# Performance work log

Hardware: AMD Instinct MI355X
Metric: run time of the kernel (lower is better)

Reference implementation:

```python
import jax, jax.numpy as jnp
import numpy as np


def setup_inputs() -> dict:
    key = jax.random.key(0)
    ks = jax.random.split(key, 12)
    B, S, D = 2, 1024, 1024       # batch, seq_len, hidden
    DF_S, DF_E, E = 2048, 512, 8   # shared ffn, expert ffn, n_experts
    W = 0.02                       # weight init scale
    x = jax.random.normal(ks[0], (B, S, D), jnp.float32)
    router_weight = jax.random.normal(ks[1], (E, D), jnp.float32) * W
    sh_gate_w = jax.random.normal(ks[2], (DF_S, D), jnp.float32) * W
    sh_up_w = jax.random.normal(ks[3], (DF_S, D), jnp.float32) * W
    sh_down_w = jax.random.normal(ks[4], (D, DF_S), jnp.float32) * W
    gate_q = jax.random.randint(ks[5], (E, DF_E, D), -128, 128, jnp.int32)
    up_q = jax.random.randint(ks[6], (E, DF_E, D), -128, 128, jnp.int32)
    down_q = jax.random.randint(ks[7], (E, D, DF_E), -128, 128, jnp.int32)
    gate_s = jax.random.uniform(ks[8], (E, DF_E), jnp.float32) * 0.001
    up_s = jax.random.uniform(ks[9], (E, DF_E), jnp.float32) * 0.001
    down_s = jax.random.uniform(ks[10], (E, D), jnp.float32) * 0.001
    alpha = 0.5 + jax.random.uniform(ks[11], (E,), jnp.float32)  # effective_alpha per expert
    return dict(x=x, router_weight=router_weight, sh_gate_w=sh_gate_w,
                sh_up_w=sh_up_w, sh_down_w=sh_down_w, gate_s=gate_s,
                up_s=up_s, down_s=down_s, alpha=alpha, gate_q=gate_q,
                up_q=up_q, down_q=down_q, top_k=2)


def reference(x, router_weight, sh_gate_w, sh_up_w, sh_down_w,
              gate_s, up_s, down_s, alpha, gate_q, up_q, down_q, top_k):
    B, S, D = x.shape
    T = B * S
    E = router_weight.shape[0]
    xf = x.reshape(T, D).astype(jnp.float32)
    # shared SwiGLU MLP
    shared = (jax.nn.silu(xf @ sh_gate_w.T) * (xf @ sh_up_w.T)) @ sh_down_w.T  # [T, D]
    # router: top-k + softmax over selected logits
    logits = xf @ router_weight.T                                # [T, E]
    k = min(int(top_k), E)
    vals, idx = jax.lax.top_k(logits, k)
    w = jax.nn.softmax(vals, axis=-1)                            # [T, k]
    # scatter routing weights into dense combine matrix [T, E] (topk idx are distinct)
    combine = jnp.zeros((T, E), jnp.float32).at[jnp.arange(T)[:, None], idx].add(w)
    # on-the-fly dequantization: int8-range quants * per-row scale
    gw = gate_q.astype(jnp.float32) * gate_s[..., None]          # [E, DF_E, D]
    uw = up_q.astype(jnp.float32) * up_s[..., None]              # [E, DF_E, D]
    dw = down_q.astype(jnp.float32) * down_s[..., None]          # [E, D, DF_E]
    # expert SwiGLU for every (token, expert) pair, combined by routing weights
    g = jnp.einsum('td,efd->tef', xf, gw)                        # [T, E, DF_E]
    u = jnp.einsum('td,efd->tef', xf, uw)
    eo = jnp.einsum('tef,edf->ted', jax.nn.silu(g) * u, dw)      # [T, E, D]
    delta = eo - shared[:, None, :]                              # expert output minus shared
    mixed = shared + jnp.einsum('te,ted->td', combine * alpha[None, :], delta)
    return mixed.reshape(B, S, D)
```

## Files before the change

kernel.cpp:

```cpp
#include <hip/hip_runtime.h>
#include <math.h>

#define T_TOK 2048
#define D_DIM 1024
#define E_NUM 8
#define DFS   2048
#define DFE   512

#define BK 32

typedef short short8 __attribute__((ext_vector_type(8)));
typedef float floatx4 __attribute__((ext_vector_type(4)));
typedef unsigned short ushort;

__device__ __forceinline__ ushort f2b(float f) {
  union { float f; unsigned u; } v; v.f = f;
  unsigned r = (v.u + 0x7fffu + ((v.u >> 16) & 1u)) >> 16;
  return (ushort)r;
}

__device__ __forceinline__ void gld16(const ushort* g, ushort* l) {
  __builtin_amdgcn_global_load_lds(
      (const __attribute__((address_space(1))) void*)g,
      (__attribute__((address_space(3))) void*)l,
      16, 0, 0);
}

__device__ __forceinline__ float silu_mul(float g, float u) {
  return (g / (1.f + __expf(-g))) * u;
}

__global__ __launch_bounds__(256) void mega_prep(
    const float* __restrict__ x, const float* __restrict__ rw,
    const float* __restrict__ alpha,
    const float* __restrict__ sg, const float* __restrict__ su,
    const float* __restrict__ sd,
    const int* __restrict__ gq, const int* __restrict__ uq,
    const int* __restrict__ dq,
    int* __restrict__ choice, float2* __restrict__ cpair,
    float* __restrict__ csum, ushort* __restrict__ xb,
    ushort* __restrict__ sgb, ushort* __restrict__ subb,
    ushort* __restrict__ sdb,
    ushort* __restrict__ gqb, ushort* __restrict__ uqb,
    ushort* __restrict__ dqb) {
  const int b = blockIdx.x;
  const int tid = threadIdx.x;
  if (b < 512) {
    __shared__ float xs[4 * D_DIM];
    const size_t base = (size_t)b * 4 * D_DIM;
#pragma unroll
    for (int j = 0; j < 4; ++j) {
      const int idx = j * 1024 + tid * 4;
      float4 v = *(const float4*)(x + base + idx);
      *(float4*)&xs[idx] = v;
      union { ushort u[4]; uint2 p; } o;
      o.u[0] = f2b(v.x); o.u[1] = f2b(v.y); o.u[2] = f2b(v.z); o.u[3] = f2b(v.w);
      *(uint2*)(xb + base + idx) = o.p;
    }
    __syncthreads();
    const int w = tid >> 6, l = tid & 63;
    const int t = b * 4 + w;
    const int e = l >> 3, sub = l & 7;
    const float* wr = rw + e * D_DIM;
    float acc = 0.f;
#pragma unroll
    for (int k = 0; k < 32; ++k) {
      const int d = k * 32 + sub * 4;
      float4 xv = *(const float4*)&xs[w * D_DIM + d];
      float4 wv = *(const float4*)(wr + d);
      acc += xv.x * wv.x + xv.y * wv.y + xv.z * wv.z + xv.w * wv.w;
    }
    acc += __shfl_xor(acc, 1);
    acc += __shfl_xor(acc, 2);
    acc += __shfl_xor(acc, 4);
    float lg[8];
#pragma unroll
    for (int i = 0; i < 8; ++i) lg[i] = __shfl(acc, i * 8);
    if (l == 0) {
      int i0 = 0; float v0 = lg[0];
#pragma unroll
      for (int i = 1; i < E_NUM; ++i) if (lg[i] > v0) { v0 = lg[i]; i0 = i; }
      int i1 = -1; float v1 = -1e30f;
#pragma unroll
      for (int i = 0; i < E_NUM; ++i) {
        if (i == i0) continue;
        if (lg[i] > v1) { v1 = lg[i]; i1 = i; }
      }
      float w0 = 1.f / (1.f + __expf(v1 - v0));
      float w1 = 1.f - w0;
      float c0 = w0 * alpha[i0];
      float c1 = w1 * alpha[i1];
      csum[t] = c0 + c1;
      choice[t] = i0 | (i1 << 4);
      cpair[t] = make_float2(c0, c1);
    }
  } else if (b < 512 + 3072) {
    const int bb = b - 512;
    const int which = bb >> 10;
    const float* src; ushort* dst;
    if (which == 0) { src = sg; dst = sgb; }
    else if (which == 1) { src = su; dst = subb; }
    else { src = sd; dst = sdb; }
    const size_t i = (size_t)(bb & 1023) * 256 + tid;
    const float4* sp = (const float4*)src;
    float4 a = sp[2 * i], c = sp[2 * i + 1];
    union { ushort u[8]; uint4 v; } o;
    o.u[0] = f2b(a.x); o.u[1] = f2b(a.y); o.u[2] = f2b(a.z); o.u[3] = f2b(a.w);
    o.u[4] = f2b(c.x); o.u[5] = f2b(c.y); o.u[6] = f2b(c.z); o.u[7] = f2b(c.w);
    ((uint4*)dst)[i] = o.v;
  } else {
    const int bb = b - 3584;
    const int which = bb >> 11;
    const int* src; ushort* dst;
    if (which == 0) { src = gq; dst = gqb; }
    else if (which == 1) { src = uq; dst = uqb; }
    else { src = dq; dst = dqb; }
    const size_t i = (size_t)(bb & 2047) * 256 + tid;
    const int4* sp = (const int4*)src;
    int4 a = sp[2 * i], c = sp[2 * i + 1];
    union { ushort u[8]; uint4 v; } o;
    o.u[0] = f2b((float)a.x); o.u[1] = f2b((float)a.y);
    o.u[2] = f2b((float)a.z); o.u[3] = f2b((float)a.w);
    o.u[4] = f2b((float)c.x); o.u[5] = f2b((float)c.y);
    o.u[6] = f2b((float)c.z); o.u[7] = f2b((float)c.w);
    ((uint4*)dst)[i] = o.v;
  }
}

__global__ __launch_bounds__(1024) void build_lists(
    const int* __restrict__ choice, int* __restrict__ cnt,
    int* __restrict__ tok_list, uint2* __restrict__ ass) {
  __shared__ int lcnt[E_NUM];
  __shared__ int lbase[E_NUM];
  const int tid = threadIdx.x;
  if (tid < E_NUM) lcnt[tid] = 0;
  __syncthreads();
  uint2 tmp[T_TOK / 1024];
#pragma unroll
  for (int r = 0; r < T_TOK / 1024; ++r) {
    const int t = r * 1024 + tid;
    const int ch = choice[t];
    const int i0 = ch & 15, i1 = ch >> 4;
    const int p0 = atomicAdd(&lcnt[i0], 1);
    tok_list[i0 * T_TOK + p0] = t;
    const int p1 = atomicAdd(&lcnt[i1], 1);
    tok_list[i1 * T_TOK + p1] = t;
    tmp[r] = make_uint2((unsigned)((i0 << 16) | p0), (unsigned)((i1 << 16) | p1));
  }
  __syncthreads();
  if (tid < E_NUM) {
    int b = 0;
    for (int i = 0; i < tid; ++i) b += lcnt[i];
    lbase[tid] = b;
    cnt[tid] = lcnt[tid];
    cnt[8 + tid] = b;
  }
  __syncthreads();
#pragma unroll
  for (int r = 0; r < T_TOK / 1024; ++r) {
    const int t = r * 1024 + tid;
    const uint2 v = tmp[r];
    ass[t] = make_uint2(lbase[v.x >> 16] + (v.x & 0xffffu),
                        lbase[v.y >> 16] + (v.y & 0xffffu));
  }
}

__global__ __launch_bounds__(256) void mfma_gateup_all(
    const ushort* __restrict__ xb,
    const ushort* __restrict__ wg, const ushort* __restrict__ wu,
    const ushort* __restrict__ gq, const ushort* __restrict__ uq,
    const float* __restrict__ gate_s, const float* __restrict__ up_s,
    const int* __restrict__ cnt, const int* __restrict__ tok_list,
    ushort* __restrict__ sbuf, ushort* __restrict__ act) {
  const int bid = blockIdx.x;
  const bool is_sh = (bid < 512);
  const int tid = threadIdx.x;
  const int wave = tid >> 6, lane = tid & 63;
  const int wr = wave >> 1, wc = wave & 1;
  const int srow = lane >> 2;
  const int scol = (lane & 3) * 8;
  const int K = D_DIM;

  int m0, n0, e = 0, ce = 0, ebase = 0;
  const ushort *aR0, *aR1, *g0, *u0;
  if (is_sh) {
    n0 = (bid & 31) * 64;
    m0 = (bid >> 5) * 128;
    aR0 = xb + (size_t)(m0 + wave * 16 + srow) * K + scol;
    aR1 = aR0 + (size_t)64 * K;
    g0 = wg + (size_t)(n0 + wave * 16 + srow) * K + scol;
    u0 = wu + (size_t)(n0 + wave * 16 + srow) * K + scol;
  } else {
    const int r = bid - 512;
    e = r >> 7;
    const int rr = r & 127;
    n0 = (rr & 7) * 64;
    m0 = (rr >> 3) * 128;
    ce = cnt[e];
    if (m0 >= ce) return;
    ebase = cnt[8 + e];
    const int r0 = m0 + wave * 16 + srow;
    const int r1 = r0 + 64;
    const int tk0 = (r0 < ce) ? tok_list[e * T_TOK + r0] : 0;
    const int tk1 = (r1 < ce) ? tok_list[e * T_TOK + r1] : 0;
    aR0 = xb + (size_t)tk0 * K + scol;
    aR1 = xb + (size_t)tk1 * K + scol;
    g0 = gq + (size_t)e * DFE * D_DIM + (size_t)(n0 + wave * 16 + srow) * K + scol;
    u0 = uq + (size_t)e * DFE * D_DIM + (size_t)(n0 + wave * 16 + srow) * K + scol;
  }

  __shared__ ushort As[2 * 128 * BK];
  __shared__ ushort Bg[2 * 64 * BK];
  __shared__ ushort Bu[2 * 64 * BK];
  ushort* lA = &As[(wave * 16) * BK];
  ushort* lG = &Bg[(wave * 16) * BK];
  ushort* lU = &Bu[(wave * 16) * BK];

  floatx4 accg[4][2], accu[4][2];
#pragma unroll
  for (int i = 0; i < 4; ++i)
#pragma unroll
    for (int j = 0; j < 2; ++j) { accg[i][j] = (floatx4)(0.f); accu[i][j] = (floatx4)(0.f); }

  const int kc = (lane >> 4) * 8;
  const int rb = lane & 15;

  for (int k0 = 0; k0 < K; k0 += 64) {
#pragma unroll
    for (int h = 0; h < 2; ++h) {
      gld16(aR0 + k0 + h * BK, lA + h * 128 * BK);
      gld16(aR1 + k0 + h * BK, lA + h * 128 * BK + 64 * BK);
      gld16(g0 + k0 + h * BK, lG + h * 64 * BK);
      gld16(u0 + k0 + h * BK, lU + h * 64 * BK);
    }
    __syncthreads();
#pragma unroll
    for (int h = 0; h < 2; ++h) {
      const int hoA = h * 128 * BK;
      const int hoB = h * 64 * BK;
      short8 af[4], gf[2], uf[2];
#pragma unroll
      for (int mt = 0; mt < 4; ++mt)
        af[mt] = *(const short8*)&As[hoA + (wr * 64 + mt * 16 + rb) * BK + kc];
#pragma unroll
      for (int nt = 0; nt < 2; ++nt) {
        gf[nt] = *(const short8*)&Bg[hoB + (wc * 32 + nt * 16 + rb) * BK + kc];
        uf[nt] = *(const short8*)&Bu[hoB + (wc * 32 + nt * 16 + rb) * BK + kc];
      }
#pragma unroll
      for (int mt = 0; mt < 4; ++mt)
#pragma unroll
        for (int nt = 0; nt < 2; ++nt) {
          accg[mt][nt] = __builtin_amdgcn_mfma_f32_16x16x32_bf16(af[mt], gf[nt], accg[mt][nt], 0, 0, 0);
          accu[mt][nt] = __builtin_amdgcn_mfma_f32_16x16x32_bf16(af[mt], uf[nt], accu[mt][nt], 0, 0, 0);
        }
    }
    __syncthreads();
  }

  if (is_sh) {
#pragma unroll
    for (int mt = 0; mt < 4; ++mt)
#pragma unroll
      for (int nt = 0; nt < 2; ++nt) {
        const int col = n0 + wc * 32 + nt * 16 + rb;
#pragma unroll
        for (int r = 0; r < 4; ++r) {
          const int row = m0 + wr * 64 + mt * 16 + (lane >> 4) * 4 + r;
          float s = silu_mul(accg[mt][nt][r], accu[mt][nt][r]);
          sbuf[(size_t)row * DFS + col] = f2b(s);
        }
      }
  } else {
#pragma unroll
    for (int mt = 0; mt < 4; ++mt)
#pragma unroll
      for (int nt = 0; nt < 2; ++nt) {
        const int col = n0 + wc * 32 + nt * 16 + rb;
        const float gsc = gate_s[e * DFE + col];
        const float usc = up_s[e * DFE + col];
#pragma unroll
        for (int r = 0; r < 4; ++r) {
          const int slot = m0 + wr * 64 + mt * 16 + (lane >> 4) * 4 + r;
          if (slot < ce) {
            float s = silu_mul(accg[mt][nt][r] * gsc, accu[mt][nt][r] * usc);
            act[(size_t)(ebase + slot) * DFE + col] = f2b(s);
          }
        }
      }
  }
}

__global__ __launch_bounds__(256) void mfma_down_all(
    const ushort* __restrict__ sb, const ushort* __restrict__ wd,
    const ushort* __restrict__ act, const ushort* __restrict__ dq,
    const float* __restrict__ down_s, const int* __restrict__ cnt,
    float* __restrict__ shd0, float* __restrict__ shd1,
    float* __restrict__ pbuf) {
  const int bid = blockIdx.x;
  const bool is_sh = (bid < 256);
  const int tid = threadIdx.x;
  const int wave = tid >> 6, lane = tid & 63;
  const int wr = wave >> 1, wc = wave & 1;
  const int srow = lane >> 2;
  const int scol = (lane & 3) * 8;

  int m0, n0, e = 0, ce = 0, ebase = 0, klen;
  const ushort *aR0, *aR1, *bR0, *bR1;
  float* dst;
  if (is_sh) {
    const int z = bid >> 7;
    const int rr = bid & 127;
    n0 = (rr & 7) * 128;
    m0 = (rr >> 3) * 128;
    const int kb = z * (DFS / 2);
    klen = DFS / 2;
    dst = z ? shd1 : shd0;
    aR0 = sb + (size_t)(m0 + wave * 16 + srow) * DFS + kb + scol;
    aR1 = aR0 + (size_t)64 * DFS;
    bR0 = wd + (size_t)(n0 + wave * 16 + srow) * DFS + kb + scol;
    bR1 = bR0 + (size_t)64 * DFS;
  } else {
    const int r = bid - 256;
    e = r >> 7;
    const int rr = r & 127;
    n0 = (rr & 7) * 128;
    m0 = (rr >> 3) * 128;
    ce = cnt[e];
    if (m0 >= ce) return;
    ebase = cnt[8 + e];
    klen = DFE;
    dst = pbuf;
    aR0 = act + (size_t)(ebase + m0 + wave * 16 + srow) * DFE + scol;
    aR1 = aR0 + (size_t)64 * DFE;
    bR0 = dq + (size_t)e * D_DIM * DFE + (size_t)(n0 + wave * 16 + srow) * DFE + scol;
    bR1 = bR0 + (size_t)64 * DFE;
  }

  __shared__ ushort As[2 * 128 * BK];
  __shared__ ushort Bs[2 * 128 * BK];
  ushort* lA = &As[(wave * 16) * BK];
  ushort* lB = &Bs[(wave * 16) * BK];

  floatx4 acc[4][4];
#pragma unroll
  for (int i = 0; i < 4; ++i)
#pragma unroll
    for (int j = 0; j < 4; ++j) acc[i][j] = (floatx4)(0.f);

  const int kc = (lane >> 4) * 8;
  const int rb = lane & 15;

  for (int k0 = 0; k0 < klen; k0 += 64) {
#pragma unroll
    for (int h = 0; h < 2; ++h) {
      gld16(aR0 + k0 + h * BK, lA + h * 128 * BK);
      gld16(aR1 + k0 + h * BK, lA + h * 128 * BK + 64 * BK);
      gld16(bR0 + k0 + h * BK, lB + h * 128 * BK);
      gld16(bR1 + k0 + h * BK, lB + h * 128 * BK + 64 * BK);
    }
    __syncthreads();
#pragma unroll
    for (int h = 0; h < 2; ++h) {
      const int ho = h * 128 * BK;
      short8 af[4], bf[4];
#pragma unroll
      for (int mt = 0; mt < 4; ++mt)
        af[mt] = *(const short8*)&As[ho + (wr * 64 + mt * 16 + rb) * BK + kc];
#pragma unroll
      for (int nt = 0; nt < 4; ++nt)
        bf[nt] = *(const short8*)&Bs[ho + (wc * 64 + nt * 16 + rb) * BK + kc];
#pragma unroll
      for (int mt = 0; mt < 4; ++mt)
#pragma unroll
        for (int nt = 0; nt < 4; ++nt)
          acc[mt][nt] = __builtin_amdgcn_mfma_f32_16x16x32_bf16(af[mt], bf[nt], acc[mt][nt], 0, 0, 0);
    }
    __syncthreads();
  }

  if (is_sh) {
#pragma unroll
    for (int mt = 0; mt < 4; ++mt)
#pragma unroll
      for (int nt = 0; nt < 4; ++nt) {
        const int col = n0 + wc * 64 + nt * 16 + rb;
#pragma unroll
        for (int r = 0; r < 4; ++r) {
          const int row = m0 + wr * 64 + mt * 16 + (lane >> 4) * 4 + r;
          dst[(size_t)row * D_DIM + col] = acc[mt][nt][r];
        }
      }
  } else {
#pragma unroll
    for (int mt = 0; mt < 4; ++mt)
#pragma unroll
      for (int nt = 0; nt < 4; ++nt) {
        const int col = n0 + wc * 64 + nt * 16 + rb;
        const float dsc = down_s[e * D_DIM + col];
#pragma unroll
        for (int r = 0; r < 4; ++r) {
          const int slot = m0 + wr * 64 + mt * 16 + (lane >> 4) * 4 + r;
          if (slot < ce)
            dst[(size_t)(ebase + slot) * D_DIM + col] = acc[mt][nt][r] * dsc;
        }
      }
  }
}

__global__ __launch_bounds__(256) void combine_kernel(
    const float* __restrict__ shd0, const float* __restrict__ shd1,
    const float* __restrict__ pbuf, const float* __restrict__ csum,
    const float2* __restrict__ cpair, const uint2* __restrict__ ass,
    float* __restrict__ out) {
  const int t = blockIdx.x;
  const int c4 = threadIdx.x * 4;
  const float cs = 1.f - csum[t];
  const float2 cp = cpair[t];
  const uint2 a = ass[t];
  const size_t idx = (size_t)t * D_DIM + c4;
  float4 s0 = *(const float4*)(shd0 + idx);
  float4 s1 = *(const float4*)(shd1 + idx);
  float4 e0 = *(const float4*)(pbuf + (size_t)a.x * D_DIM + c4);
  float4 e1 = *(const float4*)(pbuf + (size_t)a.y * D_DIM + c4);
  float4 o;
  o.x = cs * (s0.x + s1.x) + cp.x * e0.x + cp.y * e1.x;
  o.y = cs * (s0.y + s1.y) + cp.x * e0.y + cp.y * e1.y;
  o.z = cs * (s0.z + s1.z) + cp.x * e0.z + cp.y * e1.z;
  o.w = cs * (s0.w + s1.w) + cp.x * e0.w + cp.y * e1.w;
  *(float4*)(out + idx) = o;
}

extern "C" void kernel_launch(void* const* d_in, const int* in_sizes, int n_in,
                              void* d_out, int out_size, void* d_ws, size_t ws_size,
                              hipStream_t stream) {
  const float* x         = (const float*)d_in[0];
  const float* rw        = (const float*)d_in[1];
  const float* sh_gate_w = (const float*)d_in[2];
  const float* sh_up_w   = (const float*)d_in[3];
  const float* sh_down_w = (const float*)d_in[4];
  const float* gate_s    = (const float*)d_in[5];
  const float* up_s      = (const float*)d_in[6];
  const float* down_s    = (const float*)d_in[7];
  const float* alpha     = (const float*)d_in[8];
  const int*   gate_q    = (const int*)d_in[9];
  const int*   up_q      = (const int*)d_in[10];
  const int*   down_q    = (const int*)d_in[11];

  char* ws = (char*)d_ws;
  const size_t MB = 1u << 20;
  int*    cnt      = (int*)ws;
  int*    tok_list = (int*)(ws + 1024);
  float*  csum     = (float*)(ws + 66560);
  int*    choice   = (int*)(ws + 74752);
  float2* cpair    = (float2*)(ws + 82944);
  uint2*  ass      = (uint2*)(ws + 99328);
  ushort* xb      = (ushort*)(ws + 1 * MB);
  ushort* sgb     = (ushort*)(ws + 5 * MB);
  ushort* sub     = (ushort*)(ws + 9 * MB);
  float*  shd0    = (float*)(ws + 5 * MB);
  ushort* sbuf    = (ushort*)(ws + 13 * MB);
  ushort* sdb     = (ushort*)(ws + 21 * MB);
  ushort* gqb     = (ushort*)(ws + 25 * MB);
  ushort* uqb     = (ushort*)(ws + 33 * MB);
  float*  pbuf    = (float*)(ws + 25 * MB);
  ushort* dqb     = (ushort*)(ws + 41 * MB);
  ushort* act     = (ushort*)(ws + 49 * MB);
  float*  shd1    = (float*)(ws + 53 * MB);

  float* out = (float*)d_out;

  mega_prep<<<9728, 256, 0, stream>>>(
      x, rw, alpha, sh_gate_w, sh_up_w, sh_down_w, gate_q, up_q, down_q,
      choice, cpair, csum, xb, sgb, sub, sdb, gqb, uqb, dqb);
  build_lists<<<1, 1024, 0, stream>>>(choice, cnt, tok_list, ass);

  mfma_gateup_all<<<512 + 1024, 256, 0, stream>>>(
      xb, sgb, sub, gqb, uqb, gate_s, up_s, cnt, tok_list, sbuf, act);
  mfma_down_all<<<256 + 1024, 256, 0, stream>>>(
      sbuf, sdb, act, dqb, down_s, cnt, shd0, shd1, pbuf);
  combine_kernel<<<T_TOK, 256, 0, stream>>>(shd0, shd1, pbuf, csum, cpair, ass, out);
}
```

Baseline: 226.2 us.

## Double-buffer LDS tiles to prefetch next K chunk during MFMA compute

Both GEMM main loops now stage one BK-wide K chunk per iteration into alternating LDS buffers. The next chunk's async global-to-LDS loads are issued before the current chunk's MFMAs, with one barrier per iteration. Previously both halves were loaded, then a barrier, then compute, so memory latency was exposed. This aims to hide load latency behind compute, at the cost of twice as many loop iterations and barriers with less work in each.

```diff
diff --git a/kernel.cpp b/kernel.cpp
--- a/kernel.cpp
+++ b/kernel.cpp
@@ -225,38 +225,42 @@
   const int kc = (lane >> 4) * 8;
   const int rb = lane & 15;
 
-  for (int k0 = 0; k0 < K; k0 += 64) {
-#pragma unroll
-    for (int h = 0; h < 2; ++h) {
-      gld16(aR0 + k0 + h * BK, lA + h * 128 * BK);
-      gld16(aR1 + k0 + h * BK, lA + h * 128 * BK + 64 * BK);
-      gld16(g0 + k0 + h * BK, lG + h * 64 * BK);
-      gld16(u0 + k0 + h * BK, lU + h * 64 * BK);
+#define STAGE_GU(bu, ks)                                   \
+  do {                                                     \
+    gld16(aR0 + (ks), lA + (bu) * 128 * BK);               \
+    gld16(aR1 + (ks), lA + (bu) * 128 * BK + 64 * BK);     \
+    gld16(g0 + (ks), lG + (bu) * 64 * BK);                 \
+    gld16(u0 + (ks), lU + (bu) * 64 * BK);                 \
+  } while (0)
+
+  const int NK = K / BK;
+  STAGE_GU(0, 0);
+  __syncthreads();
+
+  for (int k = 0; k < NK; ++k) {
+    const int cur = k & 1;
+    if (k + 1 < NK) STAGE_GU(cur ^ 1, (k + 1) * BK);
+    const int boA = cur * 128 * BK;
+    const int boB = cur * 64 * BK;
+    short8 af[4], gf[2], uf[2];
+#pragma unroll
+    for (int mt = 0; mt < 4; ++mt)
+      af[mt] = *(const short8*)&As[boA + (wr * 64 + mt * 16 + rb) * BK + kc];
+#pragma unroll
+    for (int nt = 0; nt < 2; ++nt) {
+      gf[nt] = *(const short8*)&Bg[boB + (wc * 32 + nt * 16 + rb) * BK + kc];
+      uf[nt] = *(const short8*)&Bu[boB + (wc * 32 + nt * 16 + rb) * BK + kc];
     }
+#pragma unroll
+    for (int mt = 0; mt < 4; ++mt)
+#pragma unroll
+      for (int nt = 0; nt < 2; ++nt) {
+        accg[mt][nt] = __builtin_amdgcn_mfma_f32_16x16x32_bf16(af[mt], gf[nt], accg[mt][nt], 0, 0, 0);
+        accu[mt][nt] = __builtin_amdgcn_mfma_f32_16x16x32_bf16(af[mt], uf[nt], accu[mt][nt], 0, 0, 0);
+      }
     __syncthreads();
-#pragma unroll
-    for (int h = 0; h < 2; ++h) {
-      const int hoA = h * 128 * BK;
-      const int hoB = h * 64 * BK;
-      short8 af[4], gf[2], uf[2];
-#pragma unroll
-      for (int mt = 0; mt < 4; ++mt)
-        af[mt] = *(const short8*)&As[hoA + (wr * 64 + mt * 16 + rb) * BK + kc];
-#pragma unroll
-      for (int nt = 0; nt < 2; ++nt) {
-        gf[nt] = *(const short8*)&Bg[hoB + (wc * 32 + nt * 16 + rb) * BK + kc];
-        uf[nt] = *(const short8*)&Bu[hoB + (wc * 32 + nt * 16 + rb) * BK + kc];
-      }
-#pragma unroll
-      for (int mt = 0; mt < 4; ++mt)
-#pragma unroll
-        for (int nt = 0; nt < 2; ++nt) {
-          accg[mt][nt] = __builtin_amdgcn_mfma_f32_16x16x32_bf16(af[mt], gf[nt], accg[mt][nt], 0, 0, 0);
-          accu[mt][nt] = __builtin_amdgcn_mfma_f32_16x16x32_bf16(af[mt], uf[nt], accu[mt][nt], 0, 0, 0);
-        }
-    }
-    __syncthreads();
-  }
+  }
+#undef STAGE_GU
 
   if (is_sh) {
 #pragma unroll
@@ -351,33 +355,37 @@
   const int kc = (lane >> 4) * 8;
   const int rb = lane & 15;
 
-  for (int k0 = 0; k0 < klen; k0 += 64) {
-#pragma unroll
-    for (int h = 0; h < 2; ++h) {
-      gld16(aR0 + k0 + h * BK, lA + h * 128 * BK);
-      gld16(aR1 + k0 + h * BK, lA + h * 128 * BK + 64 * BK);
-      gld16(bR0 + k0 + h * BK, lB + h * 128 * BK);
-      gld16(bR1 + k0 + h * BK, lB + h * 128 * BK + 64 * BK);
-    }
+#define STAGE_DN(bu, ks)                                   \
+  do {                                                     \
+    gld16(aR0 + (ks), lA + (bu) * 128 * BK);               \
+    gld16(aR1 + (ks), lA + (bu) * 128 * BK + 64 * BK);     \
+    gld16(bR0 + (ks), lB + (bu) * 128 * BK);               \
+    gld16(bR1 + (ks), lB + (bu) * 128 * BK + 64 * BK);     \
+  } while (0)
+
+  const int NK = klen / BK;
+  STAGE_DN(0, 0);
+  __syncthreads();
+
+  for (int k = 0; k < NK; ++k) {
+    const int cur = k & 1;
+    if (k + 1 < NK) STAGE_DN(cur ^ 1, (k + 1) * BK);
+    const int bo = cur * 128 * BK;
+    short8 af[4], bf[4];
+#pragma unroll
+    for (int mt = 0; mt < 4; ++mt)
+      af[mt] = *(const short8*)&As[bo + (wr * 64 + mt * 16 + rb) * BK + kc];
+#pragma unroll
+    for (int nt = 0; nt < 4; ++nt)
+      bf[nt] = *(const short8*)&Bs[bo + (wc * 64 + nt * 16 + rb) * BK + kc];
+#pragma unroll
+    for (int mt = 0; mt < 4; ++mt)
+#pragma unroll
+      for (int nt = 0; nt < 4; ++nt)
+        acc[mt][nt] = __builtin_amdgcn_mfma_f32_16x16x32_bf16(af[mt], bf[nt], acc[mt][nt], 0, 0, 0);
     __syncthreads();
-#pragma unroll
-    for (int h = 0; h < 2; ++h) {
-      const int ho = h * 128 * BK;
-      short8 af[4], bf[4];
-#pragma unroll
-      for (int mt = 0; mt < 4; ++mt)
-        af[mt] = *(const short8*)&As[ho + (wr * 64 + mt * 16 + rb) * BK + kc];
-#pragma unroll
-      for (int nt = 0; nt < 4; ++nt)
-        bf[nt] = *(const short8*)&Bs[ho + (wc * 64 + nt * 16 + rb) * BK + kc];
-#pragma unroll
-      for (int mt = 0; mt < 4; ++mt)
-#pragma unroll
-        for (int nt = 0; nt < 4; ++nt)
-          acc[mt][nt] = __builtin_amdgcn_mfma_f32_16x16x32_bf16(af[mt], bf[nt], acc[mt][nt], 0, 0, 0);
-    }
-    __syncthreads();
-  }
+  }
+#undef STAGE_DN
 
   if (is_sh) {
 #pragma unroll
```

New measurement: 232.2 us. +2.6%, slower.
